# Kernel tuning notes

Hardware: AMD Instinct MI355X
Metric: run time of the kernel (lower is better)

Reference implementation:

```python
import jax, jax.numpy as jnp
import numpy as np

B, T, R, D = 16, 128, 9, 512


def _conv2d(x, w, b, pad):
    # x: [N, Cin, H, W], w: [Cout, Cin, kh, kw]
    y = jax.lax.conv_general_dilated(
        x, w, window_strides=(1, 1), padding=((pad, pad), (pad, pad)),
        dimension_numbers=('NCHW', 'OIHW', 'NCHW'))
    return y + b[None, :, None, None]


def _maxpool2(x):
    # MaxPool2d((2,2), stride=2), VALID
    return jax.lax.reduce_window(x, -jnp.inf, jax.lax.max,
                                 (1, 1, 2, 2), (1, 1, 2, 2), 'VALID')


def _f2f_similarity(q, t, qm, tm):
    # q: [B,Tq,R,D], t: [B,Tt,R,D] -> frame-to-frame Chamfer sim [B,Tq,Tt]
    sim = jnp.einsum('biok,bjpk->biopj', q, t)        # [B,Tq,R,R,Tt]
    sim = jnp.mean(jnp.max(sim, axis=3), axis=2)      # max over p, mean over o
    sim_mask = qm[:, :, None] * tm[:, None, :]        # [B,Tq,Tt]
    sim = jnp.where(sim_mask > 0, sim, 0.0)
    return sim, sim_mask


def _visil_head(sim, mask, c1w, c1b, c2w, c2b, c3w, c3b, fw, fb):
    x = sim[:, None]                                   # [N,1,T,T]
    x = jax.nn.relu(_conv2d(x, c1w, c1b, 1))
    x = _maxpool2(x)
    x = jax.nn.relu(_conv2d(x, c2w, c2b, 1))
    x = _maxpool2(x)
    x = jax.nn.relu(_conv2d(x, c3w, c3b, 1))
    x = _conv2d(x, fw, fb, 0)                          # 1x1 conv
    m = _maxpool2(_maxpool2(mask[:, None]))
    return x[:, 0], m[:, 0]                            # [N,T/4,T/4] each


def _v2v_similarity(s, mask):
    # masked Chamfer: max over axis 2, mean over axis 1
    m = jnp.max(jnp.where(mask > 0, s, -jnp.inf), axis=2)   # [N,I]
    mmax = jnp.max(mask, axis=2)                             # [N,I]
    m = jnp.where(mmax > 0, m, 0.0)
    return jnp.sum(m, axis=1) / jnp.sum(mmax, axis=1)        # [N]


def setup_inputs() -> dict:
    key = jax.random.key(0)
    ks = jax.random.split(key, 8)
    s = 0.05
    return {
        'anchors': jax.random.normal(ks[0], (B, T, R, D), jnp.float32),
        'positives': jax.random.normal(ks[1], (B, T, R, D), jnp.float32),
        'negatives': jax.random.normal(ks[2], (B, T, R, D), jnp.float32),
        'anchors_masks': jnp.ones((B, T), jnp.float32),
        'positive_masks': jnp.ones((B, T), jnp.float32),
        'negative_masks': jnp.ones((B, T), jnp.float32),
        'conv1_w': jax.random.normal(ks[3], (32, 1, 3, 3), jnp.float32) * s,
        'conv1_b': jnp.zeros((32,), jnp.float32),
        'conv2_w': jax.random.normal(ks[4], (64, 32, 3, 3), jnp.float32) * s,
        'conv2_b': jnp.zeros((64,), jnp.float32),
        'conv3_w': jax.random.normal(ks[5], (128, 64, 3, 3), jnp.float32) * s,
        'conv3_b': jnp.zeros((128,), jnp.float32),
        'fconv_w': jax.random.normal(ks[6], (1, 128, 1, 1), jnp.float32) * s,
        'fconv_b': jnp.zeros((1,), jnp.float32),
    }


def reference(anchors, positives, negatives, anchors_masks, positive_masks,
              negative_masks, conv1_w, conv1_b, conv2_w, conv2_b, conv3_w,
              conv3_b, fconv_w, fconv_b):
    pos_sim, pos_mask = _f2f_similarity(anchors, positives, anchors_masks, positive_masks)
    neg_sim, neg_mask = _f2f_similarity(anchors, negatives, anchors_masks, negative_masks)
    sim = jnp.concatenate([pos_sim, neg_sim], axis=0)        # [2B,T,T]
    sim_mask = jnp.concatenate([pos_mask, neg_mask], axis=0)
    sim, sim_mask = _visil_head(sim, sim_mask, conv1_w, conv1_b, conv2_w,
                                conv2_b, conv3_w, conv3_b, fconv_w, fconv_b)
    # SimilarityRegularizationLoss(min_val=-1, max_val=1)
    loss = jnp.sum(jax.nn.relu(-1.0 - sim)) + jnp.sum(jax.nn.relu(sim - 1.0))
    sim = jnp.clip(sim, -1.0, 1.0)                           # Hardtanh
    v = _v2v_similarity(sim, sim_mask)[:, None]              # [2B,1]
    pos_pair, neg_pair = v[:B], v[B:]
    return pos_pair, neg_pair, loss
```

## Files before the change

### kernel.cpp

```cpp
#include <hip/hip_runtime.h>
#include <float.h>
#include <cstdint>

#define BB 16
#define TT 128
#define RG 9
#define DD 512

typedef _Float16 half8 __attribute__((ext_vector_type(8)));
typedef float f32x4 __attribute__((ext_vector_type(4)));

__global__ __launch_bounds__(256) void k_wprep(
    const float* __restrict__ w2, const float* __restrict__ w3,
    _Float16* __restrict__ w2h, _Float16* __restrict__ w3h)
{
    const int e = blockIdx.x * 256 + threadIdx.x;
    if (e < 18432) {
        const int oc = e / 288, rem = e - oc * 288;
        const int ic = rem / 9, t = rem - ic * 9;
        w2h[(oc * 9 + t) * 32 + ic] = (_Float16)w2[e];
    } else if (e < 18432 + 73728) {
        const int e2 = e - 18432;
        const int oc = e2 / 576, rem = e2 - oc * 576;
        const int ic = rem / 9, t = rem - ic * 9;
        w3h[(oc * 9 + t) * 64 + ic] = (_Float16)w3[e2];
    }
}

__global__ __launch_bounds__(256) void k_pack(
    const float* __restrict__ a, const float* __restrict__ p,
    const float* __restrict__ n,
    _Float16* __restrict__ da, _Float16* __restrict__ dp,
    _Float16* __restrict__ dn)
{
    const int which = blockIdx.y;
    const float* __restrict__ s = (which == 0) ? a : (which == 1) ? p : n;
    _Float16* __restrict__ d    = (which == 0) ? da : (which == 1) ? dp : dn;
    const int tid = threadIdx.x;
    const int lane = tid & 63, wave = tid >> 6;
    const int f = blockIdx.x * 4 + wave;
    const int kc = f & 15;
    const int o  = (f >> 4) % 9;
    const int tl = (f / 144) & 7;
    const int b  = f / 1152;
    const int lo = lane & 15, hi = lane >> 4;
    const int row = tl * 16 + lo;
    const float* g = s + ((size_t)((b * TT + row) * RG + o)) * DD + kc * 32 + hi * 8;
    const float4 v0 = *reinterpret_cast<const float4*>(g);
    const float4 v1 = *reinterpret_cast<const float4*>(g + 4);
    half8 h;
    h[0] = (_Float16)v0.x; h[1] = (_Float16)v0.y;
    h[2] = (_Float16)v0.z; h[3] = (_Float16)v0.w;
    h[4] = (_Float16)v1.x; h[5] = (_Float16)v1.y;
    h[6] = (_Float16)v1.z; h[7] = (_Float16)v1.w;
    *reinterpret_cast<half8*>(d + (size_t)f * 512 + lane * 8) = h;
}

__global__ __launch_bounds__(192) void k_f2f_mfma(
    const _Float16* __restrict__ q16,
    const _Float16* __restrict__ p16,
    const _Float16* __restrict__ n16,
    const float* __restrict__ amask,
    const float* __restrict__ pmask,
    const float* __restrict__ nmask,
    float* __restrict__ simbuf)
{
    __shared__ float red[768];

    const int tid = threadIdx.x;
    const int lane = tid & 63, wave = tid >> 6;
    const int lo = lane & 15, hi = lane >> 4;

    const int hw = blockIdx.x;
    const int L  = (hw & 7) * 256 + (hw >> 3);
    const int tb = L >> 6;
    const int it = (L >> 3) & 7;
    const int jt = L & 7;

    const int b = tb & 15;
    const _Float16* __restrict__ tptr = (tb < BB) ? p16 : n16;
    const float* __restrict__ tmk  = (tb < BB) ? pmask : nmask;
    const int i0 = it * 16, j0 = jt * 16;

    const _Float16* __restrict__ qtile = q16  + (size_t)(b * 8 + it) * 73728 + lane * 8;
    const _Float16* __restrict__ ttile = tptr + (size_t)(b * 8 + jt) * 73728 + lane * 8;

    const int o0 = wave * 3;
    const _Float16* __restrict__ qp0 = qtile + (size_t)(o0 + 0) * 8192;
    const _Float16* __restrict__ qp1 = qtile + (size_t)(o0 + 1) * 8192;
    const _Float16* __restrict__ qp2 = qtile + (size_t)(o0 + 2) * 8192;

    f32x4 acc[3][9];
#pragma unroll
    for (int oi = 0; oi < 3; ++oi)
#pragma unroll
        for (int p = 0; p < 9; ++p)
            acc[oi][p] = (f32x4){0.f, 0.f, 0.f, 0.f};

    for (int ci = 0; ci < 16; ++ci) {
        const half8 a0 = *reinterpret_cast<const half8*>(qp0 + ci * 512);
        const half8 a1 = *reinterpret_cast<const half8*>(qp1 + ci * 512);
        const half8 a2 = *reinterpret_cast<const half8*>(qp2 + ci * 512);
#pragma unroll
        for (int p = 0; p < 9; ++p) {
            const half8 bf = *reinterpret_cast<const half8*>(
                ttile + (size_t)p * 8192 + ci * 512);
            acc[0][p] = __builtin_amdgcn_mfma_f32_16x16x32_f16(a0, bf, acc[0][p], 0, 0, 0);
            acc[1][p] = __builtin_amdgcn_mfma_f32_16x16x32_f16(a1, bf, acc[1][p], 0, 0, 0);
            acc[2][p] = __builtin_amdgcn_mfma_f32_16x16x32_f16(a2, bf, acc[2][p], 0, 0, 0);
        }
    }

    f32x4 part = {0.f, 0.f, 0.f, 0.f};
#pragma unroll
    for (int oi = 0; oi < 3; ++oi) {
        f32x4 m = acc[oi][0];
#pragma unroll
        for (int p = 1; p < 9; ++p) {
            m[0] = fmaxf(m[0], acc[oi][p][0]);
            m[1] = fmaxf(m[1], acc[oi][p][1]);
            m[2] = fmaxf(m[2], acc[oi][p][2]);
            m[3] = fmaxf(m[3], acc[oi][p][3]);
        }
        part[0] += m[0]; part[1] += m[1]; part[2] += m[2]; part[3] += m[3];
    }

    *reinterpret_cast<f32x4*>(red + (size_t)(wave * 64 + lane) * 4) = part;
    __syncthreads();
    if (wave == 0) {
        const f32x4 t0 = *reinterpret_cast<const f32x4*>(red + (size_t)lane * 4);
        const f32x4 t1 = *reinterpret_cast<const f32x4*>(red + (size_t)(64 + lane) * 4);
        const f32x4 t2 = *reinterpret_cast<const f32x4*>(red + (size_t)(128 + lane) * 4);
        const int j = j0 + lo;
        const float tm = tmk[b * TT + j];
#pragma unroll
        for (int r = 0; r < 4; ++r) {
            const int i = i0 + hi * 4 + r;
            const float mk = amask[b * TT + i] * tm;
            const float s = (t0[r] + t1[r] + t2[r]) * (1.f / 9.f);
            simbuf[((size_t)tb * TT + i) * TT + j] = (mk > 0.f) ? s : 0.f;
        }
    }
}

__global__ __launch_bounds__(256) void k_conv1pool(
    const float* __restrict__ simbuf, const float* __restrict__ w1,
    const float* __restrict__ b1, _Float16* __restrict__ p1pad)
{
    __shared__ float wl[288];
    __shared__ float bl[32];
    const int tid = threadIdx.x;
    const int tb = blockIdx.y, yg = blockIdx.x;
    for (int e = tid; e < 288; e += 256) wl[e] = w1[e];
    if (tid < 32)  bl[tid] = b1[tid];
    __syncthreads();

    const int y = yg * 4 + (tid >> 6);
    const int x = tid & 63;
    const float* __restrict__ sp = simbuf + (size_t)tb * TT * TT;

    float iv[4][4];
#pragma unroll
    for (int r = 0; r < 4; ++r) {
        const int gy = 2 * y - 1 + r;
#pragma unroll
        for (int c = 0; c < 4; ++c) {
            const int gx = 2 * x - 1 + c;
            iv[r][c] = (gy >= 0 && gy < TT && gx >= 0 && gx < TT)
                           ? sp[gy * TT + gx] : 0.f;
        }
    }
    _Float16 hv[32];
#pragma unroll
    for (int oc = 0; oc < 32; ++oc) {
        float a00 = 0.f, a01 = 0.f, a10 = 0.f, a11 = 0.f;
#pragma unroll
        for (int rr = 0; rr < 3; ++rr)
#pragma unroll
            for (int cc = 0; cc < 3; ++cc) {
                const float w = wl[oc * 9 + rr * 3 + cc];
                a00 = fmaf(w, iv[rr][cc],         a00);
                a01 = fmaf(w, iv[rr][cc + 1],     a01);
                a10 = fmaf(w, iv[rr + 1][cc],     a10);
                a11 = fmaf(w, iv[rr + 1][cc + 1], a11);
            }
        float m = fmaxf(fmaxf(a00, a01), fmaxf(a10, a11)) + bl[oc];
        hv[oc] = (_Float16)fmaxf(m, 0.f);
    }
    _Float16* dst = p1pad + (((size_t)tb * 66 + 1 + y) * 66 + 1 + x) * 32;
#pragma unroll
    for (int g = 0; g < 4; ++g)
        *reinterpret_cast<half8*>(dst + g * 8) = *reinterpret_cast<const half8*>(hv + g * 8);
}

__global__ __launch_bounds__(1024) void k_conv2_mfma(
    const _Float16* __restrict__ p1pad, const _Float16* __restrict__ w2h,
    const float* __restrict__ b2, _Float16* __restrict__ p2pad)
{
    __shared__ _Float16 lds[1056 * 8];
    const int tid = threadIdx.x;
    const int lane = tid & 63, widx = tid >> 6;
    const int lo = lane & 15, hi = lane >> 4;
    const int Y = blockIdx.x, tb = blockIdx.y;
    const int xh = widx & 3, oct = widx >> 2;
    const int oc0 = oct * 16;
    const int y0 = 2 * Y;

    for (int u = tid; u < 1056; u += 1024) {
        const int R = u >> 2, h = u & 3;
        const int r = R / 66, col = R - r * 66;
        const half8 v = *reinterpret_cast<const half8*>(
            p1pad + (((size_t)tb * 66 + y0 + r) * 66 + col) * 32 + h * 8);
        const int phys = (R << 2) | (h ^ (R & 3));
        *reinterpret_cast<half8*>(lds + phys * 8) = v;
    }

    half8 wf[9];
    const _Float16* wb = w2h + (size_t)(oc0 + lo) * 288 + hi * 8;
#pragma unroll
    for (int t = 0; t < 9; ++t)
        wf[t] = *reinterpret_cast<const half8*>(wb + t * 32);

    __syncthreads();

    f32x4 acc0 = {0.f, 0.f, 0.f, 0.f};
    f32x4 acc1 = {0.f, 0.f, 0.f, 0.f};
#pragma unroll
    for (int dy = 0; dy < 3; ++dy) {
#pragma unroll
        for (int dx = 0; dx < 3; ++dx) {
            const int col = xh * 16 + dx + lo;
            const int R0 = dy * 66 + col;
            const int R1 = (dy + 1) * 66 + col;
            const half8 a0 = *reinterpret_cast<const half8*>(
                lds + (((R0 << 2) | (hi ^ (R0 & 3))) * 8));
            const half8 a1 = *reinterpret_cast<const half8*>(
                lds + (((R1 << 2) | (hi ^ (R1 & 3))) * 8));
            const half8 w = wf[dy * 3 + dx];
            acc0 = __builtin_amdgcn_mfma_f32_16x16x32_f16(a0, w, acc0, 0, 0, 0);
            acc1 = __builtin_amdgcn_mfma_f32_16x16x32_f16(a1, w, acc1, 0, 0, 0);
        }
    }
    const float bias = b2[oc0 + lo];
    float p0 = fmaxf(fmaxf(acc0[0], acc0[1]), fmaxf(acc1[0], acc1[1]));
    float p1v = fmaxf(fmaxf(acc0[2], acc0[3]), fmaxf(acc1[2], acc1[3]));
    p0  = fmaxf(p0 + bias, 0.f);
    p1v = fmaxf(p1v + bias, 0.f);
    const int xo = xh * 8 + 2 * hi;
    _Float16* dst = p2pad + (((size_t)tb * 34 + 1 + Y) * 34 + 1 + xo) * 64 + oc0 + lo;
    dst[0]  = (_Float16)p0;
    dst[64] = (_Float16)p1v;
}

__global__ __launch_bounds__(1024) void k_conv3_mfma(
    const _Float16* __restrict__ p2pad, const _Float16* __restrict__ w3h,
    const float* __restrict__ b3, float* __restrict__ c3t)
{
    __shared__ _Float16 lds[816 * 8];
    const int tid = threadIdx.x;
    const int lane = tid & 63, widx = tid >> 6;
    const int lo = lane & 15, hi = lane >> 4;
    const int y = blockIdx.x, tb = blockIdx.y;
    const int xh = widx & 1, oct = widx >> 1;
    const int oc0 = oct * 16;

    if (tid < 816) {
        const int R = tid >> 3, h = tid & 7;
        const int r = R / 34, col = R - r * 34;
        const half8 v = *reinterpret_cast<const half8*>(
            p2pad + (((size_t)tb * 34 + y + r) * 34 + col) * 64 + h * 8);
        const int phys = (R << 3) | (h ^ (R & 7));
        *reinterpret_cast<half8*>(lds + phys * 8) = v;
    }

    half8 wf0[9], wf1[9];
    const _Float16* wb = w3h + (size_t)(oc0 + lo) * 576 + hi * 8;
#pragma unroll
    for (int t = 0; t < 9; ++t) {
        wf0[t] = *reinterpret_cast<const half8*>(wb + t * 64);
        wf1[t] = *reinterpret_cast<const half8*>(wb + t * 64 + 32);
    }

    __syncthreads();

    f32x4 acc = {0.f, 0.f, 0.f, 0.f};
#pragma unroll
    for (int dy = 0; dy < 3; ++dy) {
#pragma unroll
        for (int dx = 0; dx < 3; ++dx) {
            const int col = xh * 16 + dx + lo;
            const int R = dy * 34 + col;
            const half8 a0 = *reinterpret_cast<const half8*>(
                lds + (((R << 3) | (hi ^ (R & 7))) * 8));
            const half8 a1 = *reinterpret_cast<const half8*>(
                lds + (((R << 3) | ((hi + 4) ^ (R & 7))) * 8));
            acc = __builtin_amdgcn_mfma_f32_16x16x32_f16(a0, wf0[dy * 3 + dx], acc, 0, 0, 0);
            acc = __builtin_amdgcn_mfma_f32_16x16x32_f16(a1, wf1[dy * 3 + dx], acc, 0, 0, 0);
        }
    }
    const float bias = b3[oc0 + lo];
    float* dst = c3t + (((size_t)tb * 32 + y) * 32 + xh * 16 + 4 * hi) * 128 + oc0 + lo;
#pragma unroll
    for (int r = 0; r < 4; ++r)
        dst[(size_t)r * 128] = fmaxf(acc[r] + bias, 0.f);
}

__global__ __launch_bounds__(256) void k_final(
    const float* __restrict__ c3t, const float* __restrict__ fw,
    const float* __restrict__ fb, const float* __restrict__ amask,
    const float* __restrict__ pmask, const float* __restrict__ nmask,
    float* __restrict__ out, float* __restrict__ lossp)
{
    __shared__ __align__(16) float fwl[128];
    __shared__ float qmax4[32], tmax4[32];
    __shared__ float sval[1024];
    __shared__ float red[256];
    __shared__ float rowv[32], rowm[32];
    const int tid = threadIdx.x, tb = blockIdx.x;
    const int b = tb & 15;
    const float* __restrict__ tmk = (tb < BB) ? pmask : nmask;

    if (tid < 128) fwl[tid] = fw[tid];
    if (tid < 32) {
        const float* qp = amask + b * TT + 4 * tid;
        qmax4[tid] = fmaxf(fmaxf(qp[0], qp[1]), fmaxf(qp[2], qp[3]));
        const float* tp = tmk + b * TT + 4 * tid;
        tmax4[tid] = fmaxf(fmaxf(tp[0], tp[1]), fmaxf(tp[2], tp[3]));
    }
    __syncthreads();

    const float fbv = fb[0];
    float lt = 0.f;
    for (int l = 0; l < 4; ++l) {
        const int loc = tid + 256 * l;
        const int y = loc >> 5, x = loc & 31;
        const float* __restrict__ pc = c3t + ((size_t)(tb * 32 + y) * 32 + x) * 128;
        float s = fbv;
        for (int c4 = 0; c4 < 128; c4 += 4) {
            const float4 wv = *reinterpret_cast<const float4*>(&fwl[c4]);
            const float4 cv = *reinterpret_cast<const float4*>(&pc[c4]);
            s += wv.x * cv.x + wv.y * cv.y + wv.z * cv.z + wv.w * cv.w;
        }
        lt += fmaxf(0.f, -1.f - s) + fmaxf(0.f, s - 1.f);
        const float sc = fminf(fmaxf(s, -1.f), 1.f);
        const float m = qmax4[y] * tmax4[x];
        sval[loc] = (m > 0.f) ? sc : -FLT_MAX;
    }
    red[tid] = lt;
    __syncthreads();
    for (int off = 128; off > 0; off >>= 1) {
        if (tid < off) red[tid] += red[tid + off];
        __syncthreads();
    }
    if (tid == 0) lossp[tb] = red[0];

    if (tid < 32) {
        const int y = tid;
        float rm = -FLT_MAX, mm = -FLT_MAX;
        for (int x = 0; x < 32; ++x) {
            const float m = qmax4[y] * tmax4[x];
            mm = fmaxf(mm, m);
            if (m > 0.f) rm = fmaxf(rm, sval[y * 32 + x]);
        }
        rowv[y] = (mm > 0.f) ? rm : 0.f;
        rowm[y] = mm;
    }
    __syncthreads();
    if (tid == 0) {
        float num = 0.f, den = 0.f;
        for (int yy = 0; yy < 32; ++yy) { num += rowv[yy]; den += rowm[yy]; }
        out[tb] = num / den;
    }
}

__global__ void k_losssum(const float* __restrict__ lossp, float* __restrict__ out)
{
    if (threadIdx.x == 0) {
        float s = 0.f;
        for (int i = 0; i < 32; ++i) s += lossp[i];
        out[32] = s;
    }
}

extern "C" void kernel_launch(void* const* d_in, const int* in_sizes, int n_in,
                              void* d_out, int out_size, void* d_ws, size_t ws_size,
                              hipStream_t stream)
{
    (void)in_sizes; (void)n_in; (void)out_size; (void)ws_size;
    const float* anchors   = (const float*)d_in[0];
    const float* positives = (const float*)d_in[1];
    const float* negatives = (const float*)d_in[2];
    const float* amask     = (const float*)d_in[3];
    const float* pmask     = (const float*)d_in[4];
    const float* nmask     = (const float*)d_in[5];
    const float* w1 = (const float*)d_in[6];
    const float* b1 = (const float*)d_in[7];
    const float* w2 = (const float*)d_in[8];
    const float* b2 = (const float*)d_in[9];
    const float* w3 = (const float*)d_in[10];
    const float* b3 = (const float*)d_in[11];
    const float* fw = (const float*)d_in[12];
    const float* fbias = (const float*)d_in[13];

    float* ws     = (float*)d_ws;
    float* simbuf = ws;
    _Float16* q16 = (_Float16*)(ws + 524288);
    _Float16* p16 = q16 + 9437184;
    _Float16* n16 = p16 + 9437184;
    _Float16* p1pad = (_Float16*)(ws + 524288);
    _Float16* p2pad = (_Float16*)(ws + 2754560);
    float* c3t    = ws + 3938304;
    _Float16* w2h = (_Float16*)(ws + 14680064);
    _Float16* w3h = (_Float16*)(ws + 14689280);
    float* lossp  = ws + 14726144;
    float* outp   = (float*)d_out;

    hipLaunchKernelGGL(k_wprep, dim3(360), dim3(256), 0, stream, w2, w3, w2h, w3h);
    hipLaunchKernelGGL(k_pack, dim3(4608, 3), dim3(256), 0, stream,
                       anchors, positives, negatives, q16, p16, n16);
    hipLaunchKernelGGL(k_f2f_mfma, dim3(2048), dim3(192), 0, stream,
                       q16, p16, n16, amask, pmask, nmask, simbuf);
    hipMemsetAsync(p1pad, 0, (size_t)4460544 * 2, stream);
    hipMemsetAsync(p2pad, 0, (size_t)2367488 * 2, stream);
    hipLaunchKernelGGL(k_conv1pool, dim3(16, 32), dim3(256), 0, stream,
                       simbuf, w1, b1, p1pad);
    hipLaunchKernelGGL(k_conv2_mfma, dim3(32, 32), dim3(1024), 0, stream,
                       p1pad, w2h, b2, p2pad);
    hipLaunchKernelGGL(k_conv3_mfma, dim3(32, 32), dim3(1024), 0, stream,
                       p2pad, w3h, b3, c3t);
    hipLaunchKernelGGL(k_final, dim3(32), dim3(256), 0, stream,
                       c3t, fw, fbias, amask, pmask, nmask, outp, lossp);
    hipLaunchKernelGGL(k_losssum, dim3(1), dim3(64), 0, stream, lossp, outp);
}
```

Before: 182.7 us.

## Fuse 1x1 conv and loss into conv3, replace padding memsets with bounds checks

The final 1x1 convolution, hardtanh and per-row regularisation loss are moved into the conv3 epilogue using wave shuffles and a small shared reduction. This avoids writing and rereading the full fp32 conv3 activation tensor. The two memsets that zeroed the padded p1/p2 buffers are replaced by bounds checks during the LDS loads in conv2 and conv3. The final kernel now only computes the masked Chamfer, and the loss sum reduces 1024 row partials. The padding interiors still appear to be written by earlier kernels, so correctness depends on those writes covering every interior cell.

Measured after the change: 160.8 us. -11.9%, faster.

```diff
diff --git a/kernel.cpp b/kernel.cpp
--- a/kernel.cpp
+++ b/kernel.cpp
@@ -209,8 +209,13 @@
     for (int u = tid; u < 1056; u += 1024) {
         const int R = u >> 2, h = u & 3;
         const int r = R / 66, col = R - r * 66;
-        const half8 v = *reinterpret_cast<const half8*>(
-            p1pad + (((size_t)tb * 66 + y0 + r) * 66 + col) * 32 + h * 8);
+        const int row = y0 + r;
+        half8 v;
+#pragma unroll
+        for (int z = 0; z < 8; ++z) v[z] = (_Float16)0.f;
+        if (row >= 1 && row <= 64 && col >= 1 && col <= 64)
+            v = *reinterpret_cast<const half8*>(
+                p1pad + (((size_t)tb * 66 + row) * 66 + col) * 32 + h * 8);
         const int phys = (R << 2) | (h ^ (R & 3));
         *reinterpret_cast<half8*>(lds + phys * 8) = v;
     }
@@ -252,11 +257,14 @@
     dst[64] = (_Float16)p1v;
 }
 
-__global__ __launch_bounds__(1024) void k_conv3_mfma(
+__global__ __launch_bounds__(1024) void k_conv3_fused(
     const _Float16* __restrict__ p2pad, const _Float16* __restrict__ w3h,
-    const float* __restrict__ b3, float* __restrict__ c3t)
+    const float* __restrict__ b3, const float* __restrict__ fw,
+    const float* __restrict__ fb, float* __restrict__ sval,
+    float* __restrict__ rowloss)
 {
     __shared__ _Float16 lds[816 * 8];
+    __shared__ float pred[8][32];
     const int tid = threadIdx.x;
     const int lane = tid & 63, widx = tid >> 6;
     const int lo = lane & 15, hi = lane >> 4;
@@ -267,8 +275,13 @@
     if (tid < 816) {
         const int R = tid >> 3, h = tid & 7;
         const int r = R / 34, col = R - r * 34;
-        const half8 v = *reinterpret_cast<const half8*>(
-            p2pad + (((size_t)tb * 34 + y + r) * 34 + col) * 64 + h * 8);
+        const int row = y + r;
+        half8 v;
+#pragma unroll
+        for (int z = 0; z < 8; ++z) v[z] = (_Float16)0.f;
+        if (row >= 1 && row <= 32 && col >= 1 && col <= 32)
+            v = *reinterpret_cast<const half8*>(
+                p2pad + (((size_t)tb * 34 + row) * 34 + col) * 64 + h * 8);
         const int phys = (R << 3) | (h ^ (R & 7));
         *reinterpret_cast<half8*>(lds + phys * 8) = v;
     }
@@ -298,29 +311,48 @@
             acc = __builtin_amdgcn_mfma_f32_16x16x32_f16(a1, wf1[dy * 3 + dx], acc, 0, 0, 0);
         }
     }
+
     const float bias = b3[oc0 + lo];
-    float* dst = c3t + (((size_t)tb * 32 + y) * 32 + xh * 16 + 4 * hi) * 128 + oc0 + lo;
+    const float fwv  = fw[oc0 + lo];
+    float part[4];
 #pragma unroll
     for (int r = 0; r < 4; ++r)
-        dst[(size_t)r * 128] = fmaxf(acc[r] + bias, 0.f);
-}
-
-__global__ __launch_bounds__(256) void k_final(
-    const float* __restrict__ c3t, const float* __restrict__ fw,
-    const float* __restrict__ fb, const float* __restrict__ amask,
+        part[r] = fmaxf(acc[r] + bias, 0.f) * fwv;
+#pragma unroll
+    for (int m = 1; m < 16; m <<= 1)
+#pragma unroll
+        for (int r = 0; r < 4; ++r)
+            part[r] += __shfl_xor(part[r], m, 64);
+    if (lo == 0) {
+#pragma unroll
+        for (int r = 0; r < 4; ++r)
+            pred[oct][xh * 16 + 4 * hi + r] = part[r];
+    }
+    __syncthreads();
+    if (widx == 0 && lane < 32) {
+        const int x = lane;
+        float s = fb[0];
+#pragma unroll
+        for (int o8 = 0; o8 < 8; ++o8) s += pred[o8][x];
+        const float lt = fmaxf(0.f, -1.f - s) + fmaxf(0.f, s - 1.f);
+        sval[((size_t)tb * 32 + y) * 32 + x] = fminf(fmaxf(s, -1.f), 1.f);
+        float l = lt;
+#pragma unroll
+        for (int m = 1; m < 32; m <<= 1) l += __shfl_xor(l, m, 64);
+        if (lane == 0) rowloss[tb * 32 + y] = l;
+    }
+}
+
+__global__ __launch_bounds__(64) void k_final(
+    const float* __restrict__ sval, const float* __restrict__ amask,
     const float* __restrict__ pmask, const float* __restrict__ nmask,
-    float* __restrict__ out, float* __restrict__ lossp)
-{
-    __shared__ __align__(16) float fwl[128];
-    __shared__ float qmax4[32], tmax4[32];
-    __shared__ float sval[1024];
-    __shared__ float red[256];
-    __shared__ float rowv[32], rowm[32];
+    float* __restrict__ out)
+{
+    __shared__ float qmax4[32], tmax4[32], rowv[32], rowm[32];
     const int tid = threadIdx.x, tb = blockIdx.x;
     const int b = tb & 15;
     const float* __restrict__ tmk = (tb < BB) ? pmask : nmask;
 
-    if (tid < 128) fwl[tid] = fw[tid];
     if (tid < 32) {
         const float* qp = amask + b * TT + 4 * tid;
         qmax4[tid] = fmaxf(fmaxf(qp[0], qp[1]), fmaxf(qp[2], qp[3]));
@@ -328,39 +360,14 @@
         tmax4[tid] = fmaxf(fmaxf(tp[0], tp[1]), fmaxf(tp[2], tp[3]));
     }
     __syncthreads();
-
-    const float fbv = fb[0];
-    float lt = 0.f;
-    for (int l = 0; l < 4; ++l) {
-        const int loc = tid + 256 * l;
-        const int y = loc >> 5, x = loc & 31;
-        const float* __restrict__ pc = c3t + ((size_t)(tb * 32 + y) * 32 + x) * 128;
-        float s = fbv;
-        for (int c4 = 0; c4 < 128; c4 += 4) {
-            const float4 wv = *reinterpret_cast<const float4*>(&fwl[c4]);
-            const float4 cv = *reinterpret_cast<const float4*>(&pc[c4]);
-            s += wv.x * cv.x + wv.y * cv.y + wv.z * cv.z + wv.w * cv.w;
-        }
-        lt += fmaxf(0.f, -1.f - s) + fmaxf(0.f, s - 1.f);
-        const float sc = fminf(fmaxf(s, -1.f), 1.f);
-        const float m = qmax4[y] * tmax4[x];
-        sval[loc] = (m > 0.f) ? sc : -FLT_MAX;
-    }
-    red[tid] = lt;
-    __syncthreads();
-    for (int off = 128; off > 0; off >>= 1) {
-        if (tid < off) red[tid] += red[tid + off];
-        __syncthreads();
-    }
-    if (tid == 0) lossp[tb] = red[0];
-
     if (tid < 32) {
         const int y = tid;
         float rm = -FLT_MAX, mm = -FLT_MAX;
+        const float* sp = sval + ((size_t)tb * 32 + y) * 32;
         for (int x = 0; x < 32; ++x) {
             const float m = qmax4[y] * tmax4[x];
             mm = fmaxf(mm, m);
-            if (m > 0.f) rm = fmaxf(rm, sval[y * 32 + x]);
+            if (m > 0.f) rm = fmaxf(rm, sp[x]);
         }
         rowv[y] = (mm > 0.f) ? rm : 0.f;
         rowm[y] = mm;
@@ -373,13 +380,19 @@
     }
 }
 
-__global__ void k_losssum(const float* __restrict__ lossp, float* __restrict__ out)
-{
-    if (threadIdx.x == 0) {
-        float s = 0.f;
-        for (int i = 0; i < 32; ++i) s += lossp[i];
-        out[32] = s;
-    }
+__global__ __launch_bounds__(256) void k_losssum(
+    const float* __restrict__ rowloss, float* __restrict__ out)
+{
+    __shared__ float red[256];
+    const int tid = threadIdx.x;
+    red[tid] = rowloss[tid] + rowloss[tid + 256] +
+               rowloss[tid + 512] + rowloss[tid + 768];
+    __syncthreads();
+    for (int off = 128; off > 0; off >>= 1) {
+        if (tid < off) red[tid] += red[tid + off];
+        __syncthreads();
+    }
+    if (tid == 0) out[32] = red[0];
 }
 
 extern "C" void kernel_launch(void* const* d_in, const int* in_sizes, int n_in,
@@ -409,10 +422,10 @@
     _Float16* n16 = p16 + 9437184;
     _Float16* p1pad = (_Float16*)(ws + 524288);
     _Float16* p2pad = (_Float16*)(ws + 2754560);
-    float* c3t    = ws + 3938304;
     _Float16* w2h = (_Float16*)(ws + 14680064);
     _Float16* w3h = (_Float16*)(ws + 14689280);
-    float* lossp  = ws + 14726144;
+    float* sval   = ws + 14726144;
+    float* rowloss= ws + 14758912;
     float* outp   = (float*)d_out;
 
     hipLaunchKernelGGL(k_wprep, dim3(360), dim3(256), 0, stream, w2, w3, w2h, w3h);
@@ -420,15 +433,13 @@
                        anchors, positives, negatives, q16, p16, n16);
     hipLaunchKernelGGL(k_f2f_mfma, dim3(2048), dim3(192), 0, stream,
                        q16, p16, n16, amask, pmask, nmask, simbuf);
-    hipMemsetAsync(p1pad, 0, (size_t)4460544 * 2, stream);
-    hipMemsetAsync(p2pad, 0, (size_t)2367488 * 2, stream);
     hipLaunchKernelGGL(k_conv1pool, dim3(16, 32), dim3(256), 0, stream,
                        simbuf, w1, b1, p1pad);
     hipLaunchKernelGGL(k_conv2_mfma, dim3(32, 32), dim3(1024), 0, stream,
                        p1pad, w2h, b2, p2pad);
-    hipLaunchKernelGGL(k_conv3_mfma, dim3(32, 32), dim3(1024), 0, stream,
-                       p2pad, w3h, b3, c3t);
-    hipLaunchKernelGGL(k_final, dim3(32), dim3(256), 0, stream,
-                       c3t, fw, fbias, amask, pmask, nmask, outp, lossp);
-    hipLaunchKernelGGL(k_losssum, dim3(1), dim3(64), 0, stream, lossp, outp);
-}
+    hipLaunchKernelGGL(k_conv3_fused, dim3(32, 32), dim3(1024), 0, stream,
+                       p2pad, w3h, b3, fw, fbias, sval, rowloss);
+    hipLaunchKernelGGL(k_final, dim3(32), dim3(64), 0, stream,
+                       sval, amask, pmask, nmask, outp);
+    hipLaunchKernelGGL(k_losssum, dim3(1), dim3(256), 0, stream, rowloss, outp);
+}
```
